# Performance work log

Hardware: AMD Instinct MI355X
Metric: run time of the kernel (lower is better)

## Reference

```python
import jax, jax.numpy as jnp
import numpy as np

NHID = 512
NCLS = 250
CHUNK = 200  # words per class (equal class_chunks), vocab = NCLS*CHUNK = 50000
N = 2048     # flattened tokens (batch*seq after masking)


def setup_inputs() -> dict:
    key = jax.random.key(0)
    k1, k2, k3, k4, k5 = jax.random.split(key, 5)
    r = 0.1  # init_weights uniform range
    x = jax.random.normal(k1, (N, NHID), dtype=jnp.float32)
    cls_idx = jax.random.randint(k2, (N,), 0, NCLS, dtype=jnp.int64)
    Wc = jax.random.uniform(k3, (NCLS, NHID), jnp.float32, -r, r)   # cls_decoder.weight
    bc = jnp.zeros((NCLS,), jnp.float32)                             # cls_decoder.bias
    Ww = jax.random.uniform(k4, (NCLS, CHUNK, NHID), jnp.float32, -r, r)  # stacked words_decoders weights
    bw = jnp.zeros((NCLS, CHUNK), jnp.float32)                       # stacked words_decoders biases
    return {"x": x, "Wc": Wc, "bc": bc, "Ww": Ww, "bw": bw, "cls_idx": cls_idx}


def reference(x, Wc, bc, Ww, bw, cls_idx):
    # Class logits for every token: cls_decoder(input)
    p_class = jnp.einsum('nh,ch->nc', x, Wc) + bc          # [N, NCLS]
    # Per-class word decoders: each token goes through the Linear of its class.
    # Equivalent to the dict-based index_select + per-class Linear in the
    # original forward (rows reordered per-token instead of grouped by class).
    Wg = Ww[cls_idx]                                       # [N, CHUNK, NHID] irregular gather
    bg = bw[cls_idx]                                       # [N, CHUNK]
    p_words = jnp.einsum('nkh,nh->nk', Wg, x) + bg         # [N, CHUNK]
    # Concatenate class and within-class logits into one array output.
    return jnp.concatenate([p_class, p_words], axis=1)     # [N, NCLS+CHUNK]
```

## Files before the change

### kernel.cpp

```cpp
#include <hip/hip_runtime.h>

#define NHID   512
#define NCLS   250
#define CHUNK  200
#define NTOK   2048
#define NOUT   450
#define NTHR   128
#define NBLK   258
#define MAXTOK 32
#define BPAD   260

typedef __attribute__((ext_vector_type(8))) short bf16x8;
typedef __attribute__((ext_vector_type(4))) float f32x4;

#define MFMA(a, b, c) __builtin_amdgcn_mfma_f32_16x16x32_bf16((a), (b), (c), 0, 0, 0)

__device__ __forceinline__ unsigned hpack(unsigned a, unsigned b) {
    return __builtin_amdgcn_perm(a, b, 0x07060302u);
}

__device__ __forceinline__ void cvt8(float4 va, float4 vb, bf16x8& h, bf16x8& l) {
    unsigned u0 = __float_as_uint(va.x), u1 = __float_as_uint(va.y);
    unsigned u2 = __float_as_uint(va.z), u3 = __float_as_uint(va.w);
    unsigned u4 = __float_as_uint(vb.x), u5 = __float_as_uint(vb.y);
    unsigned u6 = __float_as_uint(vb.z), u7 = __float_as_uint(vb.w);
    union { unsigned w[4]; bf16x8 v; } H, L;
    H.w[0] = hpack(u1, u0); H.w[1] = hpack(u3, u2);
    H.w[2] = hpack(u5, u4); H.w[3] = hpack(u7, u6);
    float r0 = va.x - __uint_as_float(u0 & 0xffff0000u);
    float r1 = va.y - __uint_as_float(u1 & 0xffff0000u);
    float r2 = va.z - __uint_as_float(u2 & 0xffff0000u);
    float r3 = va.w - __uint_as_float(u3 & 0xffff0000u);
    float r4 = vb.x - __uint_as_float(u4 & 0xffff0000u);
    float r5 = vb.y - __uint_as_float(u5 & 0xffff0000u);
    float r6 = vb.z - __uint_as_float(u6 & 0xffff0000u);
    float r7 = vb.w - __uint_as_float(u7 & 0xffff0000u);
    L.w[0] = hpack(__float_as_uint(r1), __float_as_uint(r0));
    L.w[1] = hpack(__float_as_uint(r3), __float_as_uint(r2));
    L.w[2] = hpack(__float_as_uint(r5), __float_as_uint(r4));
    L.w[3] = hpack(__float_as_uint(r7), __float_as_uint(r6));
    h = H.v; l = L.v;
}

__device__ __forceinline__ void async16(const float* g, float* lds_base) {
    __builtin_amdgcn_global_load_lds(
        (const __attribute__((address_space(1))) unsigned*)g,
        (__attribute__((address_space(3))) unsigned*)lds_base, 16, 0, 0);
}

__device__ __forceinline__ void lds_fence_wave() {
    __builtin_amdgcn_wave_barrier();
    asm volatile("s_waitcnt lgkmcnt(0)" ::: "memory");
    __builtin_amdgcn_wave_barrier();
}

__global__ __launch_bounds__(NTHR, 1)
void cbd_fused(const float* __restrict__ x,  const float* __restrict__ Wc,
               const float* __restrict__ bc, const float* __restrict__ Ww,
               const float* __restrict__ bw, const int* __restrict__ cls_idx,
               float* __restrict__ out)
{
    __shared__ short Afrag[2][16 * 64 * 8];
    __shared__ float Bbuf[2][16 * BPAD];
    __shared__ float bias_s[208];

    const int bid  = blockIdx.x;
    const int tid  = threadIdx.x;
    const int wid  = tid >> 6;
    const int lane = tid & 63;
    const int n    = lane & 15;
    const int q    = lane >> 4;

    if (wid == 1) {
        if (bid < 256) {
            const int mt = bid >> 1, hn = bid & 1;
            const float* ap = x + (size_t)(mt * 16 + n) * NHID + q * 8;
            #pragma unroll
            for (int g4 = 0; g4 < 2; ++g4) {
                const float* bp[4]; float bias[4]; int col[4]; bool rv[4];
                #pragma unroll
                for (int k = 0; k < 4; ++k) {
                    int r = (hn * 8 + g4 * 4 + k) * 16 + n;
                    rv[k] = r < NCLS;
                    int rc = rv[k] ? r : NCLS - 1;
                    bp[k]   = Wc + (size_t)rc * NHID + q * 8;
                    bias[k] = bc[rc];
                    col[k]  = rc;
                }
                f32x4 acc[4] = {{0,0,0,0},{0,0,0,0},{0,0,0,0},{0,0,0,0}};
                #pragma unroll 2
                for (int s = 0; s < 16; ++s) {
                    float4 a0 = *(const float4*)(ap + s * 32);
                    float4 a1 = *(const float4*)(ap + s * 32 + 4);
                    bf16x8 ah, al; cvt8(a0, a1, ah, al);
                    #pragma unroll
                    for (int k = 0; k < 4; ++k) {
                        float4 b0 = *(const float4*)(bp[k] + s * 32);
                        float4 b1 = *(const float4*)(bp[k] + s * 32 + 4);
                        bf16x8 bh, bl; cvt8(b0, b1, bh, bl);
                        acc[k] = MFMA(ah, bh, acc[k]);
                        acc[k] = MFMA(al, bh, acc[k]);
                        acc[k] = MFMA(ah, bl, acc[k]);
                    }
                }
                #pragma unroll
                for (int k = 0; k < 4; ++k)
                    if (rv[k]) {
                        #pragma unroll
                        for (int i = 0; i < 4; ++i)
                            out[(size_t)(mt * 16 + q * 4 + i) * NOUT + col[k]]
                                = acc[k][i] + bias[k];
                    }
            }
        }
        return;
    }

    int myvals[32];
    #pragma unroll
    for (int it = 0; it < 8; ++it) {
        int4 v = *(const int4*)&cls_idx[it * 256 + lane * 4];
        myvals[it*4+0] = v.x; myvals[it*4+1] = v.y;
        myvals[it*4+2] = v.z; myvals[it*4+3] = v.w;
    }

    int c, slotbase;
    if (bid < NCLS) {
        c = bid; slotbase = 0;
    } else {
        int* hist = (int*)&Afrag[1][0];
        for (int i = lane; i < 256; i += 64) hist[i] = 0;
        lds_fence_wave();
        #pragma unroll
        for (int j = 0; j < 32; ++j) atomicAdd(&hist[myvals[j]], 1);
        lds_fence_wave();
        int kk = bid - NCLS, found = -1, runbase = 0;
        #pragma unroll
        for (int ch = 0; ch < 4; ++ch) {
            int hv = hist[ch * 64 + lane];
            unsigned long long m = __ballot(hv > 16);
            int c2 = (int)__popcll(m);
            if (found < 0 && kk < runbase + c2) {
                unsigned long long mm = m;
                for (int t = 0; t < 8; ++t) if (t < kk - runbase) mm &= mm - 1;
                found = ch * 64 + (__ffsll((long long)mm) - 1);
            }
            runbase += c2;
        }
        lds_fence_wave();
        if (found < 0) return;
        c = found; slotbase = 16;
    }
    const float* wsrc = Ww + (size_t)c * CHUNK * NHID;

    #pragma unroll
    for (int r = 0; r < 16; ++r)
        async16(wsrc + (size_t)r * NHID + lane * 4, &Bbuf[0][r * BPAD]);
    #pragma unroll
    for (int r = 0; r < 16; ++r)
        async16(wsrc + (size_t)r * NHID + 256 + lane * 4, &Bbuf[1][r * BPAD]);

    int* toktmp = (int*)&Afrag[0][0];
    int cnt = 0;
    #pragma unroll
    for (int j = 0; j < 32; ++j) {
        int idx  = (j >> 2) * 256 + lane * 4 + (j & 3);
        bool hit = (myvals[j] == c);
        unsigned long long m = __ballot(hit);
        if (hit) {
            int pos = cnt + (int)__popcll(m & ((1ull << lane) - 1ull));
            if (pos < MAXTOK) toktmp[pos] = idx;
        }
        cnt += (int)__popcll(m);
    }
    const int cntc = cnt < MAXTOK ? cnt : MAXTOK;
    if (slotbase >= cntc) {
        asm volatile("s_waitcnt vmcnt(0)" ::: "memory");
        return;
    }
    lds_fence_wave();
    int idx_slot = slotbase + n;
    int mytokr   = toktmp[idx_slot < cntc ? idx_slot : 0];
    lds_fence_wave();

    int tkS[4]; bool msk[4];
    #pragma unroll
    for (int i = 0; i < 4; ++i) {
        int ml = q * 4 + i;
        tkS[i] = __shfl(mytokr, ml);
        msk[i] = (slotbase + ml) < cntc;
    }

    for (int i = lane; i < CHUNK; i += 64) bias_s[i] = bw[c * CHUNK + i];

    {
        int tk = __shfl(mytokr, n);
        #pragma unroll
        for (int it = 0; it < 16; ++it) {
            const float* xp = x + (size_t)tk * NHID + it * 32 + q * 8;
            float4 va = *(const float4*)xp, vb = *(const float4*)(xp + 4);
            bf16x8 hh, ll; cvt8(va, vb, hh, ll);
            int u = it * 64 + lane;
            *(bf16x8*)&Afrag[0][u * 8] = hh;
            *(bf16x8*)&Afrag[1][u * 8] = ll;
        }
    }
    lds_fence_wave();

    f32x4 acc = {0.f, 0.f, 0.f, 0.f};
    for (int hp = 0; hp < 26; ++hp) {
        if (hp < 25) asm volatile("s_waitcnt vmcnt(16)" ::: "memory");
        else         asm volatile("s_waitcnt vmcnt(0)"  ::: "memory");

        const int p = hp >> 1, h = hp & 1, buf = hp & 1;
        if (h == 0) { acc[0] = 0.f; acc[1] = 0.f; acc[2] = 0.f; acc[3] = 0.f; }
        #pragma unroll
        for (int ss = 0; ss < 8; ++ss) {
            const int sg = h * 8 + ss;
            bf16x8 ah = *(const bf16x8*)&Afrag[0][(sg * 64 + lane) * 8];
            bf16x8 al = *(const bf16x8*)&Afrag[1][(sg * 64 + lane) * 8];
            const float* bq = &Bbuf[buf][n * BPAD + ss * 32 + q * 8];
            float4 b0 = *(const float4*)bq;
            float4 b1 = *(const float4*)(bq + 4);
            bf16x8 bh, bl; cvt8(b0, b1, bh, bl);
            acc = MFMA(ah, bh, acc);
            acc = MFMA(al, bh, acc);
            acc = MFMA(ah, bl, acc);
        }

        if (h == 1) {
            int r = p * 16 + n;
            if (r < CHUNK) {
                float bias = bias_s[r];
                #pragma unroll
                for (int i = 0; i < 4; ++i)
                    if (msk[i])
                        out[(size_t)tkS[i] * NOUT + NCLS + r] = acc[i] + bias;
            }
        }

        if (hp + 2 < 26) {
            const int p2 = (hp + 2) >> 1, h2 = (hp + 2) & 1;
            const int koff = h2 * 256;
            #pragma unroll
            for (int r = 0; r < 16; ++r) {
                int rr = p2 * 16 + r; if (rr > CHUNK - 1) rr = CHUNK - 1;
                async16(wsrc + (size_t)rr * NHID + koff + lane * 4,
                        &Bbuf[buf][r * BPAD]);
            }
        }
    }
}

extern "C" void kernel_launch(void* const* d_in, const int* in_sizes, int n_in,
                              void* d_out, int out_size, void* d_ws, size_t ws_size,
                              hipStream_t stream) {
    const float* x   = (const float*)d_in[0];
    const float* Wc  = (const float*)d_in[1];
    const float* bc  = (const float*)d_in[2];
    const float* Ww  = (const float*)d_in[3];
    const float* bw  = (const float*)d_in[4];
    const int*   cls = (const int*)d_in[5];
    float* out = (float*)d_out;
    hipLaunchKernelGGL(cbd_fused, dim3(NBLK), dim3(NTHR), 0, stream,
                       x, Wc, bc, Ww, bw, cls, out);
}
```

Measured before the change: 181.4 us.

## Split word decoding into per-class panel blocks with direct global loads

Restructures the word-decoder work so each single-wave block handles one 16-row panel of one class (250×13 blocks), rather than one block streaming all 200 rows of a class through LDS with async prefetch. Tokens are looped in groups of 16, so the overflow-block histogram path goes away and classes with many tokens are handled in-block. The class-logit GEMM moves to its own separate blocks. This buys far more parallelism and occupancy, at the cost of each panel block rescanning cls_idx and reloading x rows and weights from global memory without LDS staging.

```diff
diff --git a/kernel.cpp b/kernel.cpp
--- a/kernel.cpp
+++ b/kernel.cpp
@@ -5,10 +5,12 @@
 #define CHUNK  200
 #define NTOK   2048
 #define NOUT   450
-#define NTHR   128
-#define NBLK   258
-#define MAXTOK 32
-#define BPAD   260
+#define NPAN   13
+#define NWB    (NCLS * NPAN)
+#define NCB    256
+#define NBLK   (NWB + NCB)
+#define NTHR   64
+#define MAXTOK 64
 
 typedef __attribute__((ext_vector_type(8))) short bf16x8;
 typedef __attribute__((ext_vector_type(4))) float f32x4;
@@ -42,79 +44,69 @@
     h = H.v; l = L.v;
 }
 
-__device__ __forceinline__ void async16(const float* g, float* lds_base) {
-    __builtin_amdgcn_global_load_lds(
-        (const __attribute__((address_space(1))) unsigned*)g,
-        (__attribute__((address_space(3))) unsigned*)lds_base, 16, 0, 0);
-}
-
 __device__ __forceinline__ void lds_fence_wave() {
     __builtin_amdgcn_wave_barrier();
     asm volatile("s_waitcnt lgkmcnt(0)" ::: "memory");
     __builtin_amdgcn_wave_barrier();
 }
 
-__global__ __launch_bounds__(NTHR, 1)
+__global__ __launch_bounds__(NTHR)
 void cbd_fused(const float* __restrict__ x,  const float* __restrict__ Wc,
                const float* __restrict__ bc, const float* __restrict__ Ww,
                const float* __restrict__ bw, const int* __restrict__ cls_idx,
                float* __restrict__ out)
 {
-    __shared__ short Afrag[2][16 * 64 * 8];
-    __shared__ float Bbuf[2][16 * BPAD];
-    __shared__ float bias_s[208];
-
     const int bid  = blockIdx.x;
-    const int tid  = threadIdx.x;
-    const int wid  = tid >> 6;
-    const int lane = tid & 63;
+    const int lane = threadIdx.x;
     const int n    = lane & 15;
     const int q    = lane >> 4;
 
-    if (wid == 1) {
-        if (bid < 256) {
-            const int mt = bid >> 1, hn = bid & 1;
-            const float* ap = x + (size_t)(mt * 16 + n) * NHID + q * 8;
+    if (bid >= NWB) {
+        const int pcb = bid - NWB;
+        const int mt = pcb >> 1, hn = pcb & 1;
+        const float* ap = x + (size_t)(mt * 16 + n) * NHID + q * 8;
+        #pragma unroll
+        for (int g4 = 0; g4 < 2; ++g4) {
+            const float* bp[4]; float bias[4]; int col[4]; bool rv[4];
             #pragma unroll
-            for (int g4 = 0; g4 < 2; ++g4) {
-                const float* bp[4]; float bias[4]; int col[4]; bool rv[4];
+            for (int k = 0; k < 4; ++k) {
+                int r = (hn * 8 + g4 * 4 + k) * 16 + n;
+                rv[k] = r < NCLS;
+                int rc = rv[k] ? r : NCLS - 1;
+                bp[k]   = Wc + (size_t)rc * NHID + q * 8;
+                bias[k] = bc[rc];
+                col[k]  = rc;
+            }
+            f32x4 acc[4] = {{0,0,0,0},{0,0,0,0},{0,0,0,0},{0,0,0,0}};
+            #pragma unroll 2
+            for (int s = 0; s < 16; ++s) {
+                float4 a0 = *(const float4*)(ap + s * 32);
+                float4 a1 = *(const float4*)(ap + s * 32 + 4);
+                bf16x8 ah, al; cvt8(a0, a1, ah, al);
                 #pragma unroll
                 for (int k = 0; k < 4; ++k) {
-                    int r = (hn * 8 + g4 * 4 + k) * 16 + n;
-                    rv[k] = r < NCLS;
-                    int rc = rv[k] ? r : NCLS - 1;
-                    bp[k]   = Wc + (size_t)rc * NHID + q * 8;
-                    bias[k] = bc[rc];
-                    col[k]  = rc;
+                    float4 b0 = *(const float4*)(bp[k] + s * 32);
+                    float4 b1 = *(const float4*)(bp[k] + s * 32 + 4);
+                    bf16x8 bh, bl; cvt8(b0, b1, bh, bl);
+                    acc[k] = MFMA(ah, bh, acc[k]);
+                    acc[k] = MFMA(al, bh, acc[k]);
+                    acc[k] = MFMA(ah, bl, acc[k]);
                 }
-                f32x4 acc[4] = {{0,0,0,0},{0,0,0,0},{0,0,0,0},{0,0,0,0}};
-                #pragma unroll 2
-                for (int s = 0; s < 16; ++s) {
-                    float4 a0 = *(const float4*)(ap + s * 32);
-                    float4 a1 = *(const float4*)(ap + s * 32 + 4);
-                    bf16x8 ah, al; cvt8(a0, a1, ah, al);
+            }
+            #pragma unroll
+            for (int k = 0; k < 4; ++k)
+                if (rv[k]) {
                     #pragma unroll
-                    for (int k = 0; k < 4; ++k) {
-                        float4 b0 = *(const float4*)(bp[k] + s * 32);
-                        float4 b1 = *(const float4*)(bp[k] + s * 32 + 4);
-                        bf16x8 bh, bl; cvt8(b0, b1, bh, bl);
-                        acc[k] = MFMA(ah, bh, acc[k]);
-                        acc[k] = MFMA(al, bh, acc[k]);
-                        acc[k] = MFMA(ah, bl, acc[k]);
-                    }
+                    for (int i = 0; i < 4; ++i)
+                        out[(size_t)(mt * 16 + q * 4 + i) * NOUT + col[k]]
+                            = acc[k][i] + bias[k];
                 }
-                #pragma unroll
-                for (int k = 0; k < 4; ++k)
-                    if (rv[k]) {
-                        #pragma unroll
-                        for (int i = 0; i < 4; ++i)
-                            out[(size_t)(mt * 16 + q * 4 + i) * NOUT + col[k]]
-                                = acc[k][i] + bias[k];
-                    }
-            }
         }
         return;
     }
+
+    const int c = bid / NPAN;
+    const int p = bid - c * NPAN;
 
     int myvals[32];
     #pragma unroll
@@ -123,44 +115,7 @@
         myvals[it*4+0] = v.x; myvals[it*4+1] = v.y;
         myvals[it*4+2] = v.z; myvals[it*4+3] = v.w;
     }
-
-    int c, slotbase;
-    if (bid < NCLS) {
-        c = bid; slotbase = 0;
-    } else {
-        int* hist = (int*)&Afrag[1][0];
-        for (int i = lane; i < 256; i += 64) hist[i] = 0;
-        lds_fence_wave();
-        #pragma unroll
-        for (int j = 0; j < 32; ++j) atomicAdd(&hist[myvals[j]], 1);
-        lds_fence_wave();
-        int kk = bid - NCLS, found = -1, runbase = 0;
-        #pragma unroll
-        for (int ch = 0; ch < 4; ++ch) {
-            int hv = hist[ch * 64 + lane];
-            unsigned long long m = __ballot(hv > 16);
-            int c2 = (int)__popcll(m);
-            if (found < 0 && kk < runbase + c2) {
-                unsigned long long mm = m;
-                for (int t = 0; t < 8; ++t) if (t < kk - runbase) mm &= mm - 1;
-                found = ch * 64 + (__ffsll((long long)mm) - 1);
-            }
-            runbase += c2;
-        }
-        lds_fence_wave();
-        if (found < 0) return;
-        c = found; slotbase = 16;
-    }
-    const float* wsrc = Ww + (size_t)c * CHUNK * NHID;
-
-    #pragma unroll
-    for (int r = 0; r < 16; ++r)
-        async16(wsrc + (size_t)r * NHID + lane * 4, &Bbuf[0][r * BPAD]);
-    #pragma unroll
-    for (int r = 0; r < 16; ++r)
-        async16(wsrc + (size_t)r * NHID + 256 + lane * 4, &Bbuf[1][r * BPAD]);
-
-    int* toktmp = (int*)&Afrag[0][0];
+    __shared__ int toktmp[MAXTOK];
     int cnt = 0;
     #pragma unroll
     for (int j = 0; j < 32; ++j) {
@@ -173,81 +128,47 @@
         }
         cnt += (int)__popcll(m);
     }
+    if (cnt == 0) return;
     const int cntc = cnt < MAXTOK ? cnt : MAXTOK;
-    if (slotbase >= cntc) {
-        asm volatile("s_waitcnt vmcnt(0)" ::: "memory");
-        return;
-    }
-    lds_fence_wave();
-    int idx_slot = slotbase + n;
-    int mytokr   = toktmp[idx_slot < cntc ? idx_slot : 0];
     lds_fence_wave();
 
-    int tkS[4]; bool msk[4];
-    #pragma unroll
-    for (int i = 0; i < 4; ++i) {
-        int ml = q * 4 + i;
-        tkS[i] = __shfl(mytokr, ml);
-        msk[i] = (slotbase + ml) < cntc;
-    }
+    const int r  = p * 16 + n;
+    const int rr = r < CHUNK ? r : CHUNK - 1;
+    const float* wp  = Ww + ((size_t)c * CHUNK + rr) * NHID + q * 8;
+    const float bias = bw[c * CHUNK + rr];
 
-    for (int i = lane; i < CHUNK; i += 64) bias_s[i] = bw[c * CHUNK + i];
+    for (int sb = 0; sb < cntc; sb += 16) {
+        int slot  = sb + n;
+        int mytok = toktmp[slot < cntc ? slot : 0];
+        int tkS[4]; bool msk[4];
+        #pragma unroll
+        for (int i = 0; i < 4; ++i) {
+            int m = q * 4 + i;
+            tkS[i] = __shfl(mytok, m);
+            msk[i] = (sb + m) < cntc;
+        }
+        const float* apx = x + (size_t)mytok * NHID + q * 8;
 
-    {
-        int tk = __shfl(mytokr, n);
-        #pragma unroll
-        for (int it = 0; it < 16; ++it) {
-            const float* xp = x + (size_t)tk * NHID + it * 32 + q * 8;
-            float4 va = *(const float4*)xp, vb = *(const float4*)(xp + 4);
-            bf16x8 hh, ll; cvt8(va, vb, hh, ll);
-            int u = it * 64 + lane;
-            *(bf16x8*)&Afrag[0][u * 8] = hh;
-            *(bf16x8*)&Afrag[1][u * 8] = ll;
-        }
-    }
-    lds_fence_wave();
-
-    f32x4 acc = {0.f, 0.f, 0.f, 0.f};
-    for (int hp = 0; hp < 26; ++hp) {
-        if (hp < 25) asm volatile("s_waitcnt vmcnt(16)" ::: "memory");
-        else         asm volatile("s_waitcnt vmcnt(0)"  ::: "memory");
-
-        const int p = hp >> 1, h = hp & 1, buf = hp & 1;
-        if (h == 0) { acc[0] = 0.f; acc[1] = 0.f; acc[2] = 0.f; acc[3] = 0.f; }
-        #pragma unroll
-        for (int ss = 0; ss < 8; ++ss) {
-            const int sg = h * 8 + ss;
-            bf16x8 ah = *(const bf16x8*)&Afrag[0][(sg * 64 + lane) * 8];
-            bf16x8 al = *(const bf16x8*)&Afrag[1][(sg * 64 + lane) * 8];
-            const float* bq = &Bbuf[buf][n * BPAD + ss * 32 + q * 8];
-            float4 b0 = *(const float4*)bq;
-            float4 b1 = *(const float4*)(bq + 4);
-            bf16x8 bh, bl; cvt8(b0, b1, bh, bl);
+        f32x4 acc = {0.f, 0.f, 0.f, 0.f};
+        #pragma unroll 4
+        for (int s = 0; s < 16; ++s) {
+            float4 a0 = *(const float4*)(apx + s * 32);
+            float4 a1 = *(const float4*)(apx + s * 32 + 4);
+            float4 b0 = *(const float4*)(wp + s * 32);
+            float4 b1 = *(const float4*)(wp + s * 32 + 4);
+            bf16x8 ah, al, bh, bl;
+            cvt8(a0, a1, ah, al);
+            cvt8(b0, b1, bh, bl);
             acc = MFMA(ah, bh, acc);
             acc = MFMA(al, bh, acc);
             acc = MFMA(ah, bl, acc);
         }
 
-        if (h == 1) {
-            int r = p * 16 + n;
-            if (r < CHUNK) {
-                float bias = bias_s[r];
-                #pragma unroll
-                for (int i = 0; i < 4; ++i)
-                    if (msk[i])
-                        out[(size_t)tkS[i] * NOUT + NCLS + r] = acc[i] + bias;
-            }
-        }
-
-        if (hp + 2 < 26) {
-            const int p2 = (hp + 2) >> 1, h2 = (hp + 2) & 1;
-            const int koff = h2 * 256;
+        if (r < CHUNK) {
             #pragma unroll
-            for (int r = 0; r < 16; ++r) {
-                int rr = p2 * 16 + r; if (rr > CHUNK - 1) rr = CHUNK - 1;
-                async16(wsrc + (size_t)rr * NHID + koff + lane * 4,
-                        &Bbuf[buf][r * BPAD]);
-            }
+            for (int i = 0; i < 4; ++i)
+                if (msk[i])
+                    out[(size_t)tkS[i] * NOUT + NCLS + r] = acc[i] + bias;
         }
     }
 }
```

Result: slower. 210.8 us (+16.2%).
